# Kernel tuning notes

Hardware: AMD Instinct MI355X
Metric: run time of the kernel (lower is better)

## Reference

```python
import jax, jax.numpy as jnp
import numpy as np

B, T, U = 4, 500, 100
D = 512   # d_model
H = 512   # d_hidden
L = 2     # num_layers
V = 64    # len(phonemes)


def setup_inputs() -> dict:
    key = jax.random.key(0)
    ks = jax.random.split(key, 14)
    g = lambda k, shp: (jax.random.normal(k, shp, jnp.float32) * 0.05)
    return {
        "input_ids": jax.random.randint(ks[0], (B, U), 0, V),
        "memory": jax.random.normal(ks[1], (B, T, D), jnp.float32),
        "emb": g(ks[2], (V, D)),
        # stacked per-layer LSTM params (torch layout: [4H, in], gate order i,f,g,o)
        "w_ih": g(ks[3], (L, 4 * H, D)),
        "w_hh": g(ks[4], (L, 4 * H, H)),
        "b_ih": g(ks[5], (L, 4 * H)),
        "b_hh": g(ks[6], (L, 4 * H)),
        "fc_w": g(ks[7], (D, H)),     # torch Linear [out, in]
        "fc_b": g(ks[8], (D,)),
        "jw1": g(ks[9], (H, 2 * D)),  # Joint.forward_layer
        "jb1": g(ks[10], (H,)),
        "jw2": g(ks[11], (V, H)),     # Joint.project_layer
        "jb2": g(ks[12], (V,)),
    }


def _lstm_layer(x, wi, wh, bi, bh):
    # x: [B, U, in] -> returns ([B, U, H], h_T [B,H], c_T [B,H])
    b = x.shape[0]
    h0 = jnp.zeros((b, H), x.dtype)
    c0 = jnp.zeros((b, H), x.dtype)
    bias = bi + bh

    def step(carry, xt):
        h, c = carry
        gates = xt @ wi.T + h @ wh.T + bias  # [B, 4H]
        i, f, g, o = jnp.split(gates, 4, axis=-1)
        c = jax.nn.sigmoid(f) * c + jax.nn.sigmoid(i) * jnp.tanh(g)
        h = jax.nn.sigmoid(o) * jnp.tanh(c)
        return (h, c), h

    (hT, cT), ys = jax.lax.scan(step, (h0, c0), jnp.swapaxes(x, 0, 1))
    return jnp.swapaxes(ys, 0, 1), hT, cT


def reference(input_ids, memory, emb, w_ih, w_hh, b_ih, b_hh, fc_w, fc_b, jw1, jb1, jw2, jb2):
    # embedding lookup
    x = emb[input_ids]  # [B, U, D]
    hs, cs = [], []
    for l in range(L):
        x, hT, cT = _lstm_layer(x, w_ih[l], w_hh[l], b_ih[l], b_hh[l])
        hs.append(hT)
        cs.append(cT)
    h = jnp.stack(hs)  # [L, B, H]
    c = jnp.stack(cs)
    x = x @ fc_w.T + fc_b  # [B, U, D]

    # Joint: linear over concat(enc, dec) == split-weight broadcast add (same math)
    we = jw1[:, :D]  # acts on enc_state
    wd = jw1[:, D:]  # acts on dec_state
    enc_p = jnp.einsum("btd,hd->bth", memory, we)  # [B, T, H]
    dec_p = jnp.einsum("bud,hd->buh", x, wd)       # [B, U, H]
    joint_h = jnp.tanh(enc_p[:, :, None, :] + dec_p[:, None, :, :] + jb1)  # [B,T,U,H]
    out = jnp.einsum("btuh,vh->btuv", joint_h, jw2) + jb2  # [B, T, U, V]
    return out, h, c
```

## Files before the change

### kernel.cpp

```cpp
#include <hip/hip_runtime.h>

#define Bc 4
#define Tc 500
#define Uc 100
#define Vc 64
#define G4 2048

typedef __attribute__((ext_vector_type(8))) short short8v;
typedef __attribute__((ext_vector_type(4))) float f32x4;
typedef _Float16 h2v __attribute__((ext_vector_type(2)));

__device__ __forceinline__ float fsig(float x) {
  return __builtin_amdgcn_rcpf(1.f + __expf(-x));
}
__device__ __forceinline__ float ftanh(float x) {
  float e = __expf(2.f * x);
  return 1.f - 2.f * __builtin_amdgcn_rcpf(e + 1.f);
}
__device__ __forceinline__ short f2bf(float f) {
  unsigned u = __float_as_uint(f);
  unsigned r = (u + 0x7FFFu + ((u >> 16) & 1u)) >> 16;
  return (short)r;
}

__device__ __forceinline__ unsigned ldA(const unsigned* p) {
  return __hip_atomic_load(p, __ATOMIC_RELAXED, __HIP_MEMORY_SCOPE_AGENT);
}
__device__ __forceinline__ void stA(unsigned* p, unsigned v) {
  __hip_atomic_store(p, v, __ATOMIC_RELAXED, __HIP_MEMORY_SCOPE_AGENT);
}

template <int ATOMICST>
__device__ __forceinline__ void gemm_tile(
    const float* __restrict__ A, int lda,
    const float* __restrict__ Bw, int ldb,
    const float* __restrict__ bias, const float* __restrict__ bias2,
    float* __restrict__ C, int ldc, int N, int m0, int n0,
    const int* __restrict__ ids, const float* __restrict__ emb)
{
  __shared__ float As[16][65];
  __shared__ float Bs[16][65];
  const int tid = threadIdx.x;
  const int tx = tid & 15, ty = tid >> 4;
  float acc[4][4] = {};
  for (int k0 = 0; k0 < 512; k0 += 16) {
#pragma unroll
    for (int i = 0; i < 4; ++i) {
      int n = n0 + ty + 16 * i;
      float av = 0.f;
      if (n < N) {
        const float* ar = ids ? (emb + (long)ids[n] * 512) : (A + (long)n * lda);
        av = ar[k0 + tx];
      }
      As[tx][ty + 16 * i] = av;
      Bs[tx][ty + 16 * i] = Bw[(long)(m0 + ty + 16 * i) * ldb + k0 + tx];
    }
    __syncthreads();
#pragma unroll
    for (int kl = 0; kl < 16; ++kl) {
      float a[4], b[4];
#pragma unroll
      for (int i = 0; i < 4; ++i) a[i] = As[kl][ty * 4 + i];
#pragma unroll
      for (int j = 0; j < 4; ++j) b[j] = Bs[kl][tx * 4 + j];
#pragma unroll
      for (int i = 0; i < 4; ++i)
#pragma unroll
        for (int j = 0; j < 4; ++j) acc[i][j] += a[i] * b[j];
    }
    __syncthreads();
  }
#pragma unroll
  for (int i = 0; i < 4; ++i) {
    int n = n0 + ty * 4 + i;
    if (n >= N) continue;
#pragma unroll
    for (int j = 0; j < 4; ++j) {
      int m = m0 + tx * 4 + j;
      float v = acc[i][j];
      if (bias)  v += bias[m];
      if (bias2) v += bias2[m];
      if (ATOMICST)
        stA((unsigned*)C + (long)n * ldc + m, __float_as_uint(v));
      else
        C[(long)n * ldc + m] = v;
    }
  }
}

__device__ void wdc_tile(const float* __restrict__ jw1,
                         const float* __restrict__ fc_w,
                         float* __restrict__ wdc, int n0, int m0)
{
  __shared__ float As[16][65];
  __shared__ float Bs[16][65];
  const int tid = threadIdx.x;
  const int tx = tid & 15, ty = tid >> 4;
  float acc[4][4] = {};
  for (int k0 = 0; k0 < 512; k0 += 16) {
#pragma unroll
    for (int i = 0; i < 4; ++i) {
      As[tx][ty + 16 * i] = jw1[(long)(n0 + ty + 16 * i) * 1024 + 512 + k0 + tx];
      Bs[ty][tx + 16 * i] = fc_w[(long)(k0 + ty) * 512 + m0 + tx + 16 * i];
    }
    __syncthreads();
#pragma unroll
    for (int kl = 0; kl < 16; ++kl) {
      float a[4], b[4];
#pragma unroll
      for (int i = 0; i < 4; ++i) a[i] = As[kl][ty * 4 + i];
#pragma unroll
      for (int j = 0; j < 4; ++j) b[j] = Bs[kl][tx * 4 + j];
#pragma unroll
      for (int i = 0; i < 4; ++i)
#pragma unroll
        for (int j = 0; j < 4; ++j) acc[i][j] += a[i] * b[j];
    }
    __syncthreads();
  }
#pragma unroll
  for (int i = 0; i < 4; ++i)
#pragma unroll
    for (int j = 0; j < 4; ++j)
      stA((unsigned*)wdc + (long)(n0 + ty * 4 + i) * 512 + m0 + tx * 4 + j,
          __float_as_uint(acc[i][j]));
}

__device__ void dec_tile(const float* __restrict__ h1s, const float* __restrict__ wdc,
                         const float* __restrict__ jw1, const float* __restrict__ fc_b,
                         const float* __restrict__ jb1, float* __restrict__ decb,
                         const int* __restrict__ f1, int m0, int n0)
{
  __shared__ float As[16][65];
  __shared__ float Bs[16][65];
  __shared__ float biasl[64];
  const int tid = threadIdx.x;
  const int tx = tid & 15, ty = tid >> 4;
  int u_hi = 0;
  for (int rr = 0; rr < 64; ++rr) {
    int r = n0 + rr;
    if (r < 400) { int u = r % Uc; u_hi = max(u_hi, u + 1); }
  }
  if (tid < 32)
    while ((int)ldA((const unsigned*)(f1 + tid * 16)) < u_hi)
      __builtin_amdgcn_s_sleep(8);
  if (tid < 64) {
    int m = m0 + tid;
    const float4* wp = (const float4*)(jw1 + (long)m * 1024 + 512);
    const float4* fb = (const float4*)fc_b;
    float bb = jb1[m];
#pragma unroll 8
    for (int d4 = 0; d4 < 128; ++d4) {
      float4 w = wp[d4], f = fb[d4];
      bb += w.x * f.x + w.y * f.y + w.z * f.z + w.w * f.w;
    }
    biasl[tid] = bb;
  }
  __syncthreads();
  const unsigned* h1u = (const unsigned*)h1s;
  const unsigned* wdu = (const unsigned*)wdc;
  float acc[4][4] = {};
  for (int k0 = 0; k0 < 512; k0 += 16) {
    unsigned uA[4], uB[4];
#pragma unroll
    for (int i = 0; i < 4; ++i) {
      int n = n0 + ty + 16 * i;
      uA[i] = (n < 400) ? ldA(h1u + (long)(n % Uc) * G4 + (n / Uc) * 512 + k0 + tx) : 0u;
      uB[i] = ldA(wdu + (long)(m0 + ty + 16 * i) * 512 + k0 + tx);
    }
#pragma unroll
    for (int i = 0; i < 4; ++i) {
      int n = n0 + ty + 16 * i;
      while (uA[i] == 0xFFFFFFFFu)
        uA[i] = ldA(h1u + (long)(n % Uc) * G4 + (n / Uc) * 512 + k0 + tx);
      while (uB[i] == 0xFFFFFFFFu)
        uB[i] = ldA(wdu + (long)(m0 + ty + 16 * i) * 512 + k0 + tx);
      As[tx][ty + 16 * i] = __uint_as_float(uA[i]);
      Bs[tx][ty + 16 * i] = __uint_as_float(uB[i]);
    }
    __syncthreads();
#pragma unroll
    for (int kl = 0; kl < 16; ++kl) {
      float a[4], b[4];
#pragma unroll
      for (int i = 0; i < 4; ++i) a[i] = As[kl][ty * 4 + i];
#pragma unroll
      for (int j = 0; j < 4; ++j) b[j] = Bs[kl][tx * 4 + j];
#pragma unroll
      for (int i = 0; i < 4; ++i)
#pragma unroll
        for (int j = 0; j < 4; ++j) acc[i][j] += a[i] * b[j];
    }
    __syncthreads();
  }
#pragma unroll
  for (int i = 0; i < 4; ++i) {
    int n = n0 + ty * 4 + i;
    if (n >= 400) continue;
#pragma unroll
    for (int j = 0; j < 4; ++j)
      stA((unsigned*)decb + (long)n * 512 + m0 + tx * 4 + j,
          __float_as_uint(acc[i][j] + biasl[tx * 4 + j]));
  }
}

__device__ void rec_path(
    const float* __restrict__ ixp0,
    const float* __restrict__ wih1, const float* __restrict__ whh0,
    const float* __restrict__ whh1,
    const float* __restrict__ bih1, const float* __restrict__ bhh1,
    unsigned* __restrict__ h0s16, unsigned* __restrict__ h1s16,
    float* __restrict__ h1s32,
    float* __restrict__ hO, float* __restrict__ cO, int* __restrict__ flags)
{
  __shared__ unsigned hl[2048];
  __shared__ float4 red4[512];
  const int tid = threadIdx.x;
  const int blk = blockIdx.x;
  const bool isL1 = blk >= 16;
  const int jb = blk - 16;
  const int rg = tid & 15, ks = tid >> 4;
  const int lane = tid & 63, wv = tid >> 6;
  int* f1 = flags + 512;

  h2v wr[8][16];
#pragma unroll
  for (int r = 0; r < 8; ++r) {
    int lr = rg * 8 + r;
    const float* wsrc; int grow;
    if (!isL1) { int q = lr >> 5, uu = lr & 31; grow = q * 512 + blk * 32 + uu; wsrc = whh0; }
    else {
      if (lr < 64) { int q = lr >> 4, uu = lr & 15; grow = q * 512 + jb * 16 + uu; wsrc = wih1; }
      else { int l2 = lr - 64; int q = l2 >> 4, uu = l2 & 15; grow = q * 512 + jb * 16 + uu; wsrc = whh1; }
    }
    const float* wp = wsrc + (long)grow * 512 + ks * 32;
#pragma unroll
    for (int jj = 0; jj < 16; ++jj) {
      h2v t; t[0] = (_Float16)wp[2 * jj]; t[1] = (_Float16)wp[2 * jj + 1];
      wr[r][jj] = t;
    }
  }

  const int npair = isL1 ? 8 : 16;
  const bool eact = tid < npair * 4;
  const int ep = tid >> 2, eb = tid & 3;
  float creg[2] = {0.f, 0.f};
  float bgate[2][4];
  if (isL1 && eact) {
#pragma unroll
    for (int o = 0; o < 2; ++o)
#pragma unroll
      for (int q = 0; q < 4; ++q) {
        int grow = q * 512 + jb * 16 + 2 * ep + o;
        bgate[o][q] = bih1[grow] + bhh1[grow];
      }
  }

  const unsigned* ixu = (const unsigned*)ixp0;
  const int hsrc = (isL1 && rg >= 8) ? 1 : 0;
  const float* redf = (const float*)red4;

  for (int s = 0; s < Uc; ++s) {
    unsigned ha[4] = {0u, 0u, 0u, 0u}, hb[4] = {0u, 0u, 0u, 0u};
    const unsigned* pa = nullptr; const unsigned* pb = nullptr;
    if (!isL1) { if (s > 0) pa = h0s16 + (long)(s - 1) * 1024 + tid * 4; }
    else {
      pa = h0s16 + (long)s * 1024 + tid * 4;
      if (s > 0) pb = h1s16 + (long)(s - 1) * 1024 + tid * 4;
    }
    if (pa) {
#pragma unroll
      for (int c = 0; c < 4; ++c) ha[c] = ldA(pa + c);
    }
    if (pb) {
#pragma unroll
      for (int c = 0; c < 4; ++c) hb[c] = ldA(pb + c);
    }

    float ixv[2][4] = {};
    if (!isL1 && eact) {
      const unsigned* ib = ixu + ((long)(eb * Uc + s) * G4 + blk * 32 + 2 * ep);
#pragma unroll
      for (int o = 0; o < 2; ++o)
#pragma unroll
        for (int q = 0; q < 4; ++q) {
          unsigned g = ldA(ib + o + q * 512);
          while (g == 0xFFFFFFFFu) { __builtin_amdgcn_s_sleep(1); g = ldA(ib + o + q * 512); }
          ixv[o][q] = __uint_as_float(g);
        }
    }

    if (pa) {
#pragma unroll
      for (int c = 0; c < 4; ++c)
        while (ha[c] == 0xFFFFFFFFu) { __builtin_amdgcn_s_sleep(1); ha[c] = ldA(pa + c); }
    }
    if (pb) {
#pragma unroll
      for (int c = 0; c < 4; ++c)
        while (hb[c] == 0xFFFFFFFFu) { __builtin_amdgcn_s_sleep(1); hb[c] = ldA(pb + c); }
    }

    *(uint4*)&hl[tid * 4] = make_uint4(ha[0], ha[1], ha[2], ha[3]);
    if (isL1)
      *(uint4*)&hl[1024 + tid * 4] = make_uint4(hb[0], hb[1], hb[2], hb[3]);
    __syncthreads();

    float acc[8][4] = {};
    const unsigned* hbase = &hl[hsrc * 1024 + ks * 16];
#pragma unroll
    for (int jw = 0; jw < 4; ++jw) {
      unsigned q[4][4];
#pragma unroll
      for (int b = 0; b < 4; ++b) {
        uint4 t = *(const uint4*)&hbase[b * 256 + jw * 4];
        q[b][0] = t.x; q[b][1] = t.y; q[b][2] = t.z; q[b][3] = t.w;
      }
#pragma unroll
      for (int r = 0; r < 8; ++r)
#pragma unroll
        for (int w = 0; w < 4; ++w) {
          h2v wv2 = wr[r][jw * 4 + w];
#pragma unroll
          for (int b = 0; b < 4; ++b)
            acc[r][b] = __builtin_amdgcn_fdot2(
                wv2, __builtin_bit_cast(h2v, q[b][w]), acc[r][b], false);
        }
    }
#pragma unroll
    for (int r = 0; r < 8; ++r)
#pragma unroll
      for (int b = 0; b < 4; ++b) {
        float v = acc[r][b];
        v += __shfl_xor(v, 16);
        v += __shfl_xor(v, 32);
        acc[r][b] = v;
      }
    if (lane < 16) {
#pragma unroll
      for (int r = 0; r < 8; ++r)
        red4[wv * 128 + lane * 8 + r] =
            make_float4(acc[r][0], acc[r][1], acc[r][2], acc[r][3]);
    }
    __syncthreads();

    if (eact) {
      float hn2[2], cn2[2];
#pragma unroll
      for (int o = 0; o < 2; ++o) {
        int uu = 2 * ep + o;
        float gv[4];
#pragma unroll
        for (int q = 0; q < 4; ++q) {
          int lrA = isL1 ? (q * 16 + uu) : (q * 32 + uu);
          float sv = 0.f;
#pragma unroll
          for (int w = 0; w < 4; ++w)
            sv += redf[(w * 128 + (lrA >> 3) * 8 + (lrA & 7)) * 4 + eb];
          if (isL1) {
            int lrB = 64 + q * 16 + uu;
#pragma unroll
            for (int w = 0; w < 4; ++w)
              sv += redf[(w * 128 + (lrB >> 3) * 8 + (lrB & 7)) * 4 + eb];
            sv += bgate[o][q];
          } else {
            sv += ixv[o][q];
          }
          gv[q] = sv;
        }
        float cn = fsig(gv[1]) * creg[o] + fsig(gv[0]) * ftanh(gv[2]);
        float hn = fsig(gv[3]) * ftanh(cn);
        creg[o] = cn;
        hn2[o] = hn; cn2[o] = cn;
      }
      int gu = (isL1 ? jb * 16 : blk * 32) + 2 * ep;
      h2v hp; hp[0] = (_Float16)hn2[0]; hp[1] = (_Float16)hn2[1];
      unsigned pw = __builtin_bit_cast(unsigned, hp);
      stA((isL1 ? h1s16 : h0s16) + (long)s * 1024 + eb * 256 + (gu >> 1), pw);
      if (isL1) {
        unsigned* d32 = (unsigned*)h1s32 + (long)s * G4 + eb * 512 + gu;
        stA(d32, __float_as_uint(hn2[0]));
        stA(d32 + 1, __float_as_uint(hn2[1]));
      }
      if (s == Uc - 1) {
#pragma unroll
        for (int o = 0; o < 2; ++o) {
          hO[(isL1 ? G4 : 0) + eb * 512 + gu + o] = hn2[o];
          cO[(isL1 ? G4 : 0) + eb * 512 + gu + o] = cn2[o];
        }
      }
      if (isL1 && tid == 0) stA((unsigned*)(f1 + jb * 16), (unsigned)(s + 1));
    }
  }
}

__global__ __launch_bounds__(256, 1) void k_fused(
    const int* __restrict__ ids, const float* __restrict__ emb,
    const float* __restrict__ memory,
    const float* __restrict__ w_ih, const float* __restrict__ b_ih,
    const float* __restrict__ b_hh,
    const float* __restrict__ wih1, const float* __restrict__ whh0,
    const float* __restrict__ whh1,
    const float* __restrict__ bih1, const float* __restrict__ bhh1,
    const float* __restrict__ jw1, const float* __restrict__ jb1,
    const float* __restrict__ fc_w, const float* __restrict__ fc_b,
    float* __restrict__ ixp0, unsigned* __restrict__ h0s16,
    unsigned* __restrict__ h1s16, float* __restrict__ h1s32,
    float* __restrict__ wdc, float* __restrict__ decb, float* __restrict__ encb,
    float* __restrict__ hO, float* __restrict__ cO, int* __restrict__ flags)
{
  const int blk = blockIdx.x;
  if (blk < 48) {
    rec_path(ixp0, wih1, whh0, whh1, bih1, bhh1, h0s16, h1s16, h1s32,
             hO, cO, flags);
  } else if (blk < 272) {
    static const int nt_ord[7] = {0, 1, 3, 4, 2, 5, 6};
    int g = blk - 48;
    gemm_tile<1>(nullptr, 0, w_ih, 512, b_ih, b_hh,
                 ixp0, G4, Bc * Uc, (g % 32) * 64, nt_ord[g / 32] * 64, ids, emb);
  } else if (blk < 336) {
    int g = blk - 272;
    wdc_tile(jw1, fc_w, wdc, (g & 7) * 64, (g >> 3) * 64);
  } else if (blk < 592) {
    int g = blk - 336;
    gemm_tile<0>(memory, 512, jw1, 1024, nullptr, nullptr,
                 encb, 512, Bc * Tc, (g & 7) * 64, (g >> 3) * 64, nullptr, nullptr);
  } else {
    int g = blk - 592;
    dec_tile(h1s32, wdc, jw1, fc_b, jb1, decb, flags + 512, (g & 7) * 64, (g >> 3) * 64);
  }
}

__global__ __launch_bounds__(256) void k_jmfma(
    const float* __restrict__ enc, const float* __restrict__ dec,
    const float* __restrict__ jw2, const float* __restrict__ jb2,
    float* __restrict__ out)
{
  __shared__ float el[512];
  __shared__ short th[112][136];
  const int tid = threadIdx.x;
  const int lane = tid & 63, wv = tid >> 6;
  const int bt = blockIdx.x;
  const int b = bt / Tc;
  const int v0 = wv * 16;
  const int vl = lane & 15, kg = lane >> 4;

  short8v breg[16];
#pragma unroll
  for (int ksx = 0; ksx < 16; ++ksx) {
    const float* wp = jw2 + (long)(v0 + vl) * 512 + ksx * 32 + kg * 8;
    float4 x0 = *(const float4*)wp;
    float4 x1 = *(const float4*)(wp + 4);
    short8v t;
    t[0] = f2bf(x0.x); t[1] = f2bf(x0.y); t[2] = f2bf(x0.z); t[3] = f2bf(x0.w);
    t[4] = f2bf(x1.x); t[5] = f2bf(x1.y); t[6] = f2bf(x1.z); t[7] = f2bf(x1.w);
    breg[ksx] = t;
  }
  const float jbv = jb2[v0 + vl];
  for (int i = tid; i < 512; i += 256) el[i] = enc[(long)bt * 512 + i];

  f32x4 acc[7];
#pragma unroll
  for (int ut = 0; ut < 7; ++ut) acc[ut] = (f32x4){0.f, 0.f, 0.f, 0.f};
  __syncthreads();

  const float* dec0 = dec + (long)b * Uc * 512;
  for (int kc = 0; kc < 4; ++kc) {
#pragma unroll 5
    for (int it = 0; it < 50; ++it) {
      int flat = it * 256 + tid;
      int u = flat >> 7, kk = flat & 127;
      float dv = dec0[(long)u * 512 + kc * 128 + kk];
      th[u][kk] = f2bf(ftanh(el[kc * 128 + kk] + dv));
    }
    __syncthreads();
#pragma unroll
    for (int ks4 = 0; ks4 < 4; ++ks4) {
      int ko = ks4 * 32 + kg * 8;
#pragma unroll
      for (int ut = 0; ut < 7; ++ut) {
        short8v a = *(const short8v*)&th[ut * 16 + vl][ko];
        acc[ut] = __builtin_amdgcn_mfma_f32_16x16x32_bf16(a, breg[kc * 4 + ks4],
                                                          acc[ut], 0, 0, 0);
      }
    }
    __syncthreads();
  }
#pragma unroll
  for (int ut = 0; ut < 7; ++ut) {
#pragma unroll
    for (int i = 0; i < 4; ++i) {
      int u = ut * 16 + kg * 4 + i;
      if (u < Uc)
        out[((long)bt * Uc + u) * 64 + v0 + vl] = acc[ut][i] + jbv;
    }
  }
}

extern "C" void kernel_launch(void* const* d_in, const int* in_sizes, int n_in,
                              void* d_out, int out_size, void* d_ws, size_t ws_size,
                              hipStream_t stream)
{
  const int*   ids    = (const int*)d_in[0];
  const float* memory = (const float*)d_in[1];
  const float* emb    = (const float*)d_in[2];
  const float* w_ih   = (const float*)d_in[3];
  const float* w_hh   = (const float*)d_in[4];
  const float* b_ih   = (const float*)d_in[5];
  const float* b_hh   = (const float*)d_in[6];
  const float* fc_w   = (const float*)d_in[7];
  const float* fc_b   = (const float*)d_in[8];
  const float* jw1    = (const float*)d_in[9];
  const float* jb1    = (const float*)d_in[10];
  const float* jw2    = (const float*)d_in[11];
  const float* jb2    = (const float*)d_in[12];
  float* out = (float*)d_out;

  float* wsf = (float*)d_ws;
  int*      flags = (int*)d_ws;
  float*    ixp0  = wsf + 4096;
  unsigned* h0s16 = (unsigned*)(wsf + 823296);
  unsigned* h1s16 = (unsigned*)(wsf + 925696);
  float*    h1s32 = wsf + 1028096;
  float*    wdc   = wsf + 1232896;
  float*    decb  = wsf + 1495040;
  float*    encb  = wsf + 1699840;

  float* hO = out + (long)Bc * Tc * Uc * Vc;
  float* cO = hO + 2 * Bc * 512;

  hipMemsetAsync(flags, 0, 4096 * 4, stream);
  hipMemsetAsync(ixp0, 0xFF, (size_t)(1699840 - 4096) * 4, stream);

  k_fused<<<648, 256, 0, stream>>>(ids, emb, memory,
                                   w_ih, b_ih, b_hh,
                                   w_ih + (long)G4 * 512,
                                   w_hh,
                                   w_hh + (long)G4 * 512,
                                   b_ih + G4, b_hh + G4,
                                   jw1, jb1, fc_w, fc_b,
                                   ixp0, h0s16, h1s16, h1s32, wdc, decb, encb,
                                   hO, cO, flags);

  k_jmfma<<<2000, 256, 0, stream>>>(encb, decb, jw2, jb2, out);
}
```

Baseline: 774.6 us.

## Halve recurrent LSTM block count, spill extra weight rows to shared memory

Shrinks the persistent LSTM recurrence from 48 to 24 blocks, so each block handles twice as many hidden units. Each thread now owns 16 fp16 weight rows: 10 stay in registers and 6 live in a large shared-memory buffer. Fewer blocks mean fewer participants in each cross-block step handshake, which should cut per-timestep synchronization latency. In exchange, each block does twice the per-step dot-product work and reads shared memory, and the single big shared allocation (used by every role in the fused kernel) may limit how many GEMM blocks fit on a CU.

```diff
diff --git a/kernel.cpp b/kernel.cpp
--- a/kernel.cpp
+++ b/kernel.cpp
@@ -10,6 +10,11 @@
 typedef __attribute__((ext_vector_type(4))) float f32x4;
 typedef _Float16 h2v __attribute__((ext_vector_type(2)));
 
+#define SMEM_BYTES 124416
+#define WL_WORDS_STRIDE 260
+#define HL_OFF 99840
+#define RED_OFF 108032
+
 __device__ __forceinline__ float fsig(float x) {
   return __builtin_amdgcn_rcpf(1.f + __expf(-x));
 }
@@ -32,14 +37,15 @@
 
 template <int ATOMICST>
 __device__ __forceinline__ void gemm_tile(
+    char* smem,
     const float* __restrict__ A, int lda,
     const float* __restrict__ Bw, int ldb,
     const float* __restrict__ bias, const float* __restrict__ bias2,
     float* __restrict__ C, int ldc, int N, int m0, int n0,
     const int* __restrict__ ids, const float* __restrict__ emb)
 {
-  __shared__ float As[16][65];
-  __shared__ float Bs[16][65];
+  float (*As)[65] = (float (*)[65])smem;
+  float (*Bs)[65] = (float (*)[65])(smem + 4160);
   const int tid = threadIdx.x;
   const int tx = tid & 15, ty = tid >> 4;
   float acc[4][4] = {};
@@ -88,12 +94,13 @@
   }
 }
 
-__device__ void wdc_tile(const float* __restrict__ jw1,
+__device__ void wdc_tile(char* smem,
+                         const float* __restrict__ jw1,
                          const float* __restrict__ fc_w,
                          float* __restrict__ wdc, int n0, int m0)
 {
-  __shared__ float As[16][65];
-  __shared__ float Bs[16][65];
+  float (*As)[65] = (float (*)[65])smem;
+  float (*Bs)[65] = (float (*)[65])(smem + 4160);
   const int tid = threadIdx.x;
   const int tx = tid & 15, ty = tid >> 4;
   float acc[4][4] = {};
@@ -126,14 +133,15 @@
           __float_as_uint(acc[i][j]));
 }
 
-__device__ void dec_tile(const float* __restrict__ h1s, const float* __restrict__ wdc,
+__device__ void dec_tile(char* smem,
+                         const float* __restrict__ h1s, const float* __restrict__ wdc,
                          const float* __restrict__ jw1, const float* __restrict__ fc_b,
                          const float* __restrict__ jb1, float* __restrict__ decb,
                          const int* __restrict__ f1, int m0, int n0)
 {
-  __shared__ float As[16][65];
-  __shared__ float Bs[16][65];
-  __shared__ float biasl[64];
+  float (*As)[65] = (float (*)[65])smem;
+  float (*Bs)[65] = (float (*)[65])(smem + 4160);
+  float* biasl = (float*)(smem + 8320);
   const int tid = threadIdx.x;
   const int tx = tid & 15, ty = tid >> 4;
   int u_hi = 0;
@@ -141,7 +149,7 @@
     int r = n0 + rr;
     if (r < 400) { int u = r % Uc; u_hi = max(u_hi, u + 1); }
   }
-  if (tid < 32)
+  if (tid < 16)
     while ((int)ldA((const unsigned*)(f1 + tid * 16)) < u_hi)
       __builtin_amdgcn_s_sleep(8);
   if (tid < 64) {
@@ -205,6 +213,7 @@
 }
 
 __device__ void rec_path(
+    char* smem,
     const float* __restrict__ ixp0,
     const float* __restrict__ wih1, const float* __restrict__ whh0,
     const float* __restrict__ whh1,
@@ -213,35 +222,39 @@
     float* __restrict__ h1s32,
     float* __restrict__ hO, float* __restrict__ cO, int* __restrict__ flags)
 {
-  __shared__ unsigned hl[2048];
-  __shared__ float4 red4[512];
+  unsigned* wlu = (unsigned*)smem;
+  unsigned* hl  = (unsigned*)(smem + HL_OFF);
+  float*    redf = (float*)(smem + RED_OFF);
   const int tid = threadIdx.x;
   const int blk = blockIdx.x;
-  const bool isL1 = blk >= 16;
-  const int jb = blk - 16;
+  const bool isL1 = blk >= 8;
+  const int jb = blk - 8;
   const int rg = tid & 15, ks = tid >> 4;
   const int lane = tid & 63, wv = tid >> 6;
   int* f1 = flags + 512;
 
-  h2v wr[8][16];
-#pragma unroll
-  for (int r = 0; r < 8; ++r) {
-    int lr = rg * 8 + r;
+  h2v wr[10][16];
+  unsigned* wlp = wlu + (rg * 6) * WL_WORDS_STRIDE + ks * 16;
+#pragma unroll
+  for (int r = 0; r < 16; ++r) {
+    int lr = rg * 16 + r;
     const float* wsrc; int grow;
-    if (!isL1) { int q = lr >> 5, uu = lr & 31; grow = q * 512 + blk * 32 + uu; wsrc = whh0; }
+    if (!isL1) { int q = lr >> 6, uu = lr & 63; grow = q * 512 + blk * 64 + uu; wsrc = whh0; }
     else {
-      if (lr < 64) { int q = lr >> 4, uu = lr & 15; grow = q * 512 + jb * 16 + uu; wsrc = wih1; }
-      else { int l2 = lr - 64; int q = l2 >> 4, uu = l2 & 15; grow = q * 512 + jb * 16 + uu; wsrc = whh1; }
+      int half = lr >> 7, rem = lr & 127;
+      int q = rem >> 5, uu = rem & 31;
+      grow = q * 512 + jb * 32 + uu; wsrc = half ? whh1 : wih1;
     }
     const float* wp = wsrc + (long)grow * 512 + ks * 32;
 #pragma unroll
     for (int jj = 0; jj < 16; ++jj) {
       h2v t; t[0] = (_Float16)wp[2 * jj]; t[1] = (_Float16)wp[2 * jj + 1];
-      wr[r][jj] = t;
-    }
-  }
-
-  const int npair = isL1 ? 8 : 16;
+      if (r < 10) wr[r][jj] = t;
+      else        wlp[(r - 10) * WL_WORDS_STRIDE + jj] = __builtin_bit_cast(unsigned, t);
+    }
+  }
+
+  const int npair = isL1 ? 16 : 32;
   const bool eact = tid < npair * 4;
   const int ep = tid >> 2, eb = tid & 3;
   float creg[2] = {0.f, 0.f};
@@ -251,14 +264,13 @@
     for (int o = 0; o < 2; ++o)
 #pragma unroll
       for (int q = 0; q < 4; ++q) {
-        int grow = q * 512 + jb * 16 + 2 * ep + o;
+        int grow = q * 512 + jb * 32 + 2 * ep + o;
         bgate[o][q] = bih1[grow] + bhh1[grow];
       }
   }
 
   const unsigned* ixu = (const unsigned*)ixp0;
   const int hsrc = (isL1 && rg >= 8) ? 1 : 0;
-  const float* redf = (const float*)red4;
 
   for (int s = 0; s < Uc; ++s) {
     unsigned ha[4] = {0u, 0u, 0u, 0u}, hb[4] = {0u, 0u, 0u, 0u};
@@ -279,7 +291,7 @@
 
     float ixv[2][4] = {};
     if (!isL1 && eact) {
-      const unsigned* ib = ixu + ((long)(eb * Uc + s) * G4 + blk * 32 + 2 * ep);
+      const unsigned* ib = ixu + ((long)(eb * Uc + s) * G4 + blk * 64 + 2 * ep);
 #pragma unroll
       for (int o = 0; o < 2; ++o)
 #pragma unroll
@@ -306,41 +318,48 @@
       *(uint4*)&hl[1024 + tid * 4] = make_uint4(hb[0], hb[1], hb[2], hb[3]);
     __syncthreads();
 
-    float acc[8][4] = {};
     const unsigned* hbase = &hl[hsrc * 1024 + ks * 16];
 #pragma unroll
-    for (int jw = 0; jw < 4; ++jw) {
-      unsigned q[4][4];
-#pragma unroll
-      for (int b = 0; b < 4; ++b) {
-        uint4 t = *(const uint4*)&hbase[b * 256 + jw * 4];
-        q[b][0] = t.x; q[b][1] = t.y; q[b][2] = t.z; q[b][3] = t.w;
-      }
-#pragma unroll
-      for (int r = 0; r < 8; ++r)
-#pragma unroll
-        for (int w = 0; w < 4; ++w) {
-          h2v wv2 = wr[r][jw * 4 + w];
-#pragma unroll
-          for (int b = 0; b < 4; ++b)
-            acc[r][b] = __builtin_amdgcn_fdot2(
-                wv2, __builtin_bit_cast(h2v, q[b][w]), acc[r][b], false);
+    for (int p = 0; p < 2; ++p) {
+      float acc[16][2] = {};
+#pragma unroll
+      for (int jw = 0; jw < 4; ++jw) {
+        uint4 t0 = *(const uint4*)&hbase[(2 * p) * 256 + jw * 4];
+        uint4 t1 = *(const uint4*)&hbase[(2 * p + 1) * 256 + jw * 4];
+        unsigned qb0[4] = {t0.x, t0.y, t0.z, t0.w};
+        unsigned qb1[4] = {t1.x, t1.y, t1.z, t1.w};
+#pragma unroll
+        for (int r = 0; r < 16; ++r) {
+          h2v wv2[4];
+          if (r < 10) {
+#pragma unroll
+            for (int w = 0; w < 4; ++w) wv2[w] = wr[r][jw * 4 + w];
+          } else {
+            uint4 wt = *(const uint4*)&wlp[(r - 10) * WL_WORDS_STRIDE + jw * 4];
+            wv2[0] = __builtin_bit_cast(h2v, wt.x);
+            wv2[1] = __builtin_bit_cast(h2v, wt.y);
+            wv2[2] = __builtin_bit_cast(h2v, wt.z);
+            wv2[3] = __builtin_bit_cast(h2v, wt.w);
+          }
+#pragma unroll
+          for (int w = 0; w < 4; ++w) {
+            acc[r][0] = __builtin_amdgcn_fdot2(
+                wv2[w], __builtin_bit_cast(h2v, qb0[w]), acc[r][0], false);
+            acc[r][1] = __builtin_amdgcn_fdot2(
+                wv2[w], __builtin_bit_cast(h2v, qb1[w]), acc[r][1], false);
+          }
         }
-    }
-#pragma unroll
-    for (int r = 0; r < 8; ++r)
-#pragma unroll
-      for (int b = 0; b < 4; ++b) {
-        float v = acc[r][b];
-        v += __shfl_xor(v, 16);
-        v += __shfl_xor(v, 32);
-        acc[r][b] = v;
-      }
-    if (lane < 16) {
-#pragma unroll
-      for (int r = 0; r < 8; ++r)
-        red4[wv * 128 + lane * 8 + r] =
-            make_float4(acc[r][0], acc[r][1], acc[r][2], acc[r][3]);
+      }
+#pragma unroll
+      for (int r = 0; r < 16; ++r)
+#pragma unroll
+        for (int b2 = 0; b2 < 2; ++b2) {
+          float v = acc[r][b2];
+          v += __shfl_xor(v, 16);
+          v += __shfl_xor(v, 32);
+          if (lane < 16)
+            redf[((wv * 16 + lane) * 16 + r) * 4 + 2 * p + b2] = v;
+        }
     }
     __syncthreads();
 
@@ -352,19 +371,22 @@
         float gv[4];
 #pragma unroll
         for (int q = 0; q < 4; ++q) {
-          int lrA = isL1 ? (q * 16 + uu) : (q * 32 + uu);
           float sv = 0.f;
-#pragma unroll
-          for (int w = 0; w < 4; ++w)
-            sv += redf[(w * 128 + (lrA >> 3) * 8 + (lrA & 7)) * 4 + eb];
-          if (isL1) {
-            int lrB = 64 + q * 16 + uu;
+          if (!isL1) {
+            int lr = q * 64 + uu;
 #pragma unroll
             for (int w = 0; w < 4; ++w)
-              sv += redf[(w * 128 + (lrB >> 3) * 8 + (lrB & 7)) * 4 + eb];
+              sv += redf[((w * 16 + (lr >> 4)) * 16 + (lr & 15)) * 4 + eb];
+            sv += ixv[o][q];
+          } else {
+            int lrA = q * 32 + uu;
+            int lrB = 128 + q * 32 + uu;
+#pragma unroll
+            for (int w = 0; w < 4; ++w) {
+              sv += redf[((w * 16 + (lrA >> 4)) * 16 + (lrA & 15)) * 4 + eb];
+              sv += redf[((w * 16 + (lrB >> 4)) * 16 + (lrB & 15)) * 4 + eb];
+            }
             sv += bgate[o][q];
-          } else {
-            sv += ixv[o][q];
           }
           gv[q] = sv;
         }
@@ -373,7 +395,7 @@
         creg[o] = cn;
         hn2[o] = hn; cn2[o] = cn;
       }
-      int gu = (isL1 ? jb * 16 : blk * 32) + 2 * ep;
+      int gu = (isL1 ? jb * 32 : blk * 64) + 2 * ep;
       h2v hp; hp[0] = (_Float16)hn2[0]; hp[1] = (_Float16)hn2[1];
       unsigned pw = __builtin_bit_cast(unsigned, hp);
       stA((isL1 ? h1s16 : h0s16) + (long)s * 1024 + eb * 256 + (gu >> 1), pw);
@@ -391,6 +413,7 @@
       }
       if (isL1 && tid == 0) stA((unsigned*)(f1 + jb * 16), (unsigned)(s + 1));
     }
+    __syncthreads();
   }
 }
 
@@ -409,25 +432,27 @@
     float* __restrict__ wdc, float* __restrict__ decb, float* __restrict__ encb,
     float* __restrict__ hO, float* __restrict__ cO, int* __restrict__ flags)
 {
+  __shared__ __attribute__((aligned(16))) char smem[SMEM_BYTES];
   const int blk = blockIdx.x;
-  if (blk < 48) {
-    rec_path(ixp0, wih1, whh0, whh1, bih1, bhh1, h0s16, h1s16, h1s32,
+  if (blk < 24) {
+    rec_path(smem, ixp0, wih1, whh0, whh1, bih1, bhh1, h0s16, h1s16, h1s32,
              hO, cO, flags);
-  } else if (blk < 272) {
+  } else if (blk < 248) {
     static const int nt_ord[7] = {0, 1, 3, 4, 2, 5, 6};
-    int g = blk - 48;
-    gemm_tile<1>(nullptr, 0, w_ih, 512, b_ih, b_hh,
+    int g = blk - 24;
+    gemm_tile<1>(smem, nullptr, 0, w_ih, 512, b_ih, b_hh,
                  ixp0, G4, Bc * Uc, (g % 32) * 64, nt_ord[g / 32] * 64, ids, emb);
-  } else if (blk < 336) {
-    int g = blk - 272;
-    wdc_tile(jw1, fc_w, wdc, (g & 7) * 64, (g >> 3) * 64);
-  } else if (blk < 592) {
-    int g = blk - 336;
-    gemm_tile<0>(memory, 512, jw1, 1024, nullptr, nullptr,
+  } else if (blk < 312) {
+    int g = blk - 248;
+    wdc_tile(smem, jw1, fc_w, wdc, (g & 7) * 64, (g >> 3) * 64);
+  } else if (blk < 568) {
+    int g = blk - 312;
+    gemm_tile<0>(smem, memory, 512, jw1, 1024, nullptr, nullptr,
                  encb, 512, Bc * Tc, (g & 7) * 64, (g >> 3) * 64, nullptr, nullptr);
   } else {
-    int g = blk - 592;
-    dec_tile(h1s32, wdc, jw1, fc_b, jb1, decb, flags + 512, (g & 7) * 64, (g >> 3) * 64);
+    int g = blk - 568;
+    dec_tile(smem, h1s32, wdc, jw1, fc_b, jb1, decb, flags + 512,
+             (g & 7) * 64, (g >> 3) * 64);
   }
 }
 
@@ -532,7 +557,7 @@
   hipMemsetAsync(flags, 0, 4096 * 4, stream);
   hipMemsetAsync(ixp0, 0xFF, (size_t)(1699840 - 4096) * 4, stream);
 
-  k_fused<<<648, 256, 0, stream>>>(ids, emb, memory,
+  k_fused<<<624, 256, 0, stream>>>(ids, emb, memory,
                                    w_ih, b_ih, b_hh,
                                    w_ih + (long)G4 * 512,
                                    w_hh,
```

After: 1.515 ms. 1.96x slower.

## Pin recurrent blocks to one XCD and use L2-scope loads for h exchange

Applied to the files above, without the earlier changes.

Blocks now take roles dynamically through atomic tickets and read their XCC_ID so that all 48 recurrent LSTM blocks try to land on a single XCD. When all of them share an XCD, the hidden-state exchange switches to sc0 global loads and plain volatile stores instead of agent-scope atomics, aiming to keep the per-step handoff in the shared L2 rather than going further out. The input-projection values for the next step are also prefetched into registers. The cost is a spin-wait during role assignment, and correctness depends on assumptions about cache coherence within one XCD.

```diff
diff --git a/kernel.cpp b/kernel.cpp
--- a/kernel.cpp
+++ b/kernel.cpp
@@ -28,6 +28,21 @@
 }
 __device__ __forceinline__ void stA(unsigned* p, unsigned v) {
   __hip_atomic_store(p, v, __ATOMIC_RELAXED, __HIP_MEMORY_SCOPE_AGENT);
+}
+__device__ __forceinline__ unsigned ldL2(const unsigned* p) {
+  unsigned v;
+  asm volatile("global_load_dword %0, %1, off sc0\n\ts_waitcnt vmcnt(0)"
+               : "=v"(v) : "v"(p) : "memory");
+  return v;
+}
+__device__ __forceinline__ uint4 ldL2x4(const unsigned* p) {
+  uint4 v;
+  asm volatile("global_load_dwordx4 %0, %1, off sc0\n\ts_waitcnt vmcnt(0)"
+               : "=v"(v) : "v"(p) : "memory");
+  return v;
+}
+__device__ __forceinline__ void stL2(unsigned* p, unsigned v) {
+  *(volatile unsigned*)p = v;
 }
 
 template <int ATOMICST>
@@ -205,30 +220,43 @@
 }
 
 __device__ void rec_path(
+    int role,
     const float* __restrict__ ixp0,
     const float* __restrict__ wih1, const float* __restrict__ whh0,
     const float* __restrict__ whh1,
     const float* __restrict__ bih1, const float* __restrict__ bhh1,
     unsigned* __restrict__ h0s16, unsigned* __restrict__ h1s16,
     float* __restrict__ h1s32,
-    float* __restrict__ hO, float* __restrict__ cO, int* __restrict__ flags)
+    float* __restrict__ hO, float* __restrict__ cO,
+    int* __restrict__ flags, int* __restrict__ xtab)
 {
   __shared__ unsigned hl[2048];
   __shared__ float4 red4[512];
+  __shared__ int mode_s;
   const int tid = threadIdx.x;
-  const int blk = blockIdx.x;
-  const bool isL1 = blk >= 16;
-  const int jb = blk - 16;
+  const bool isL1 = role >= 16;
+  const int jb = role - 16;
   const int rg = tid & 15, ks = tid >> 4;
   const int lane = tid & 63, wv = tid >> 6;
   int* f1 = flags + 512;
 
+  if (tid < 64) {
+    int idx = (tid < 48) ? tid : 47;
+    unsigned v = ldA((const unsigned*)(xtab + idx * 16));
+    while (v == 0u) { __builtin_amdgcn_s_sleep(4); v = ldA((const unsigned*)(xtab + idx * 16)); }
+    unsigned v0 = __shfl(v, 0);
+    unsigned long long ball = __ballot(v == v0);
+    if (tid == 0) mode_s = (ball == ~0ull) ? 1 : 0;
+  }
+  __syncthreads();
+  const bool fastm = (mode_s != 0);
+
   h2v wr[8][16];
 #pragma unroll
   for (int r = 0; r < 8; ++r) {
     int lr = rg * 8 + r;
     const float* wsrc; int grow;
-    if (!isL1) { int q = lr >> 5, uu = lr & 31; grow = q * 512 + blk * 32 + uu; wsrc = whh0; }
+    if (!isL1) { int q = lr >> 5, uu = lr & 31; grow = q * 512 + role * 32 + uu; wsrc = whh0; }
     else {
       if (lr < 64) { int q = lr >> 4, uu = lr & 15; grow = q * 512 + jb * 16 + uu; wsrc = wih1; }
       else { int l2 = lr - 64; int q = l2 >> 4, uu = l2 & 15; grow = q * 512 + jb * 16 + uu; wsrc = whh1; }
@@ -259,6 +287,16 @@
   const unsigned* ixu = (const unsigned*)ixp0;
   const int hsrc = (isL1 && rg >= 8) ? 1 : 0;
   const float* redf = (const float*)red4;
+
+  unsigned ixn[8];
+  const unsigned* ib0 = (!isL1 && eact)
+      ? ixu + ((long)(eb * Uc) * G4 + role * 32 + 2 * ep) : nullptr;
+  if (ib0) {
+#pragma unroll
+    for (int o = 0; o < 2; ++o)
+#pragma unroll
+      for (int q = 0; q < 4; ++q) ixn[o * 4 + q] = ldA(ib0 + o + q * 512);
+  }
 
   for (int s = 0; s < Uc; ++s) {
     unsigned ha[4] = {0u, 0u, 0u, 0u}, hb[4] = {0u, 0u, 0u, 0u};
@@ -268,23 +306,28 @@
       pa = h0s16 + (long)s * 1024 + tid * 4;
       if (s > 0) pb = h1s16 + (long)(s - 1) * 1024 + tid * 4;
     }
-    if (pa) {
-#pragma unroll
-      for (int c = 0; c < 4; ++c) ha[c] = ldA(pa + c);
-    }
-    if (pb) {
-#pragma unroll
-      for (int c = 0; c < 4; ++c) hb[c] = ldA(pb + c);
+    if (fastm) {
+      if (pa) { uint4 t = ldL2x4(pa); ha[0] = t.x; ha[1] = t.y; ha[2] = t.z; ha[3] = t.w; }
+      if (pb) { uint4 t = ldL2x4(pb); hb[0] = t.x; hb[1] = t.y; hb[2] = t.z; hb[3] = t.w; }
+    } else {
+      if (pa) {
+#pragma unroll
+        for (int c = 0; c < 4; ++c) ha[c] = ldA(pa + c);
+      }
+      if (pb) {
+#pragma unroll
+        for (int c = 0; c < 4; ++c) hb[c] = ldA(pb + c);
+      }
     }
 
     float ixv[2][4] = {};
-    if (!isL1 && eact) {
-      const unsigned* ib = ixu + ((long)(eb * Uc + s) * G4 + blk * 32 + 2 * ep);
+    if (ib0) {
+      const unsigned* ib = ib0 + (long)s * G4;
 #pragma unroll
       for (int o = 0; o < 2; ++o)
 #pragma unroll
         for (int q = 0; q < 4; ++q) {
-          unsigned g = ldA(ib + o + q * 512);
+          unsigned g = ixn[o * 4 + q];
           while (g == 0xFFFFFFFFu) { __builtin_amdgcn_s_sleep(1); g = ldA(ib + o + q * 512); }
           ixv[o][q] = __uint_as_float(g);
         }
@@ -293,12 +336,26 @@
     if (pa) {
 #pragma unroll
       for (int c = 0; c < 4; ++c)
-        while (ha[c] == 0xFFFFFFFFu) { __builtin_amdgcn_s_sleep(1); ha[c] = ldA(pa + c); }
+        while (ha[c] == 0xFFFFFFFFu) {
+          __builtin_amdgcn_s_sleep(1);
+          ha[c] = fastm ? ldL2(pa + c) : ldA(pa + c);
+        }
     }
     if (pb) {
 #pragma unroll
       for (int c = 0; c < 4; ++c)
-        while (hb[c] == 0xFFFFFFFFu) { __builtin_amdgcn_s_sleep(1); hb[c] = ldA(pb + c); }
+        while (hb[c] == 0xFFFFFFFFu) {
+          __builtin_amdgcn_s_sleep(1);
+          hb[c] = fastm ? ldL2(pb + c) : ldA(pb + c);
+        }
+    }
+
+    if (ib0 && s + 1 < Uc) {
+      const unsigned* ibn = ib0 + (long)(s + 1) * G4;
+#pragma unroll
+      for (int o = 0; o < 2; ++o)
+#pragma unroll
+        for (int q = 0; q < 4; ++q) ixn[o * 4 + q] = ldA(ibn + o + q * 512);
     }
 
     *(uint4*)&hl[tid * 4] = make_uint4(ha[0], ha[1], ha[2], ha[3]);
@@ -373,10 +430,11 @@
         creg[o] = cn;
         hn2[o] = hn; cn2[o] = cn;
       }
-      int gu = (isL1 ? jb * 16 : blk * 32) + 2 * ep;
+      int gu = (isL1 ? jb * 16 : role * 32) + 2 * ep;
       h2v hp; hp[0] = (_Float16)hn2[0]; hp[1] = (_Float16)hn2[1];
       unsigned pw = __builtin_bit_cast(unsigned, hp);
-      stA((isL1 ? h1s16 : h0s16) + (long)s * 1024 + eb * 256 + (gu >> 1), pw);
+      unsigned* d16 = (isL1 ? h1s16 : h0s16) + (long)s * 1024 + eb * 256 + (gu >> 1);
+      if (fastm) stL2(d16, pw); else stA(d16, pw);
       if (isL1) {
         unsigned* d32 = (unsigned*)h1s32 + (long)s * G4 + eb * 512 + gu;
         stA(d32, __float_as_uint(hn2[0]));
@@ -409,24 +467,55 @@
     float* __restrict__ wdc, float* __restrict__ decb, float* __restrict__ encb,
     float* __restrict__ hO, float* __restrict__ cO, int* __restrict__ flags)
 {
-  const int blk = blockIdx.x;
-  if (blk < 48) {
-    rec_path(ixp0, wih1, whh0, whh1, bih1, bhh1, h0s16, h1s16, h1s32,
-             hO, cO, flags);
-  } else if (blk < 272) {
+  __shared__ int role_s[2];
+  int* rec_tk = flags + 1024;
+  int* wrk_tk = flags + 1040;
+  int* xtab   = flags + 1088;
+  if (threadIdx.x == 0) {
+    unsigned xcd;
+    asm volatile("s_getreg_b32 %0, hwreg(HW_REG_XCC_ID)" : "=s"(xcd));
+    xcd &= 7u;
+    int role = -1;
+    if (xcd == 0u) {
+      int r = __hip_atomic_fetch_add(rec_tk, 1, __ATOMIC_RELAXED, __HIP_MEMORY_SCOPE_AGENT);
+      if (r < 48) role = r;
+    } else {
+      for (int it = 0; it < 64; ++it) {
+        if ((int)ldA((const unsigned*)rec_tk) >= 48) break;
+        __builtin_amdgcn_s_sleep(8);
+      }
+      if ((int)ldA((const unsigned*)rec_tk) < 48) {
+        int r = __hip_atomic_fetch_add(rec_tk, 1, __ATOMIC_RELAXED, __HIP_MEMORY_SCOPE_AGENT);
+        if (r < 48) role = r;
+      }
+    }
+    int wrk = -1;
+    if (role < 0)
+      wrk = __hip_atomic_fetch_add(wrk_tk, 1, __ATOMIC_RELAXED, __HIP_MEMORY_SCOPE_AGENT);
+    else
+      stA((unsigned*)(xtab + role * 16), xcd + 1u);
+    role_s[0] = role; role_s[1] = wrk;
+  }
+  __syncthreads();
+  const int role = role_s[0];
+  const int w = role_s[1];
+
+  if (role >= 0) {
+    rec_path(role, ixp0, wih1, whh0, whh1, bih1, bhh1, h0s16, h1s16, h1s32,
+             hO, cO, flags, xtab);
+  } else if (w < 224) {
     static const int nt_ord[7] = {0, 1, 3, 4, 2, 5, 6};
-    int g = blk - 48;
     gemm_tile<1>(nullptr, 0, w_ih, 512, b_ih, b_hh,
-                 ixp0, G4, Bc * Uc, (g % 32) * 64, nt_ord[g / 32] * 64, ids, emb);
-  } else if (blk < 336) {
-    int g = blk - 272;
+                 ixp0, G4, Bc * Uc, (w % 32) * 64, nt_ord[w / 32] * 64, ids, emb);
+  } else if (w < 288) {
+    int g = w - 224;
     wdc_tile(jw1, fc_w, wdc, (g & 7) * 64, (g >> 3) * 64);
-  } else if (blk < 592) {
-    int g = blk - 336;
+  } else if (w < 544) {
+    int g = w - 288;
     gemm_tile<0>(memory, 512, jw1, 1024, nullptr, nullptr,
                  encb, 512, Bc * Tc, (g & 7) * 64, (g >> 3) * 64, nullptr, nullptr);
-  } else {
-    int g = blk - 592;
+  } else if (w < 600) {
+    int g = w - 544;
     dec_tile(h1s32, wdc, jw1, fc_b, jb1, decb, flags + 512, (g & 7) * 64, (g >> 3) * 64);
   }
 }
```

Result: slower. 832.8 us (+7.5%).

## Persist fused-kernel worker blocks over tiles and prefetch next-step input projections

Applied to the files above, without the earlier changes.

Shrinks the fused launch from 648 blocks to 256 and has the 208 non-recurrent blocks each loop over up to three tiles (ixp GEMM, wdc, encoder GEMM, decoder). All roles now share one 86016-byte shared buffer sized to force one block per CU. The layer-0 recurrent blocks also load the next step's input-projection values early so that load latency overlaps the current step. The aim is to keep the 48 spin-waiting recurrent blocks resident while cutting per-block launch overhead and exposed load latency in the serial loop. The trade-off is less parallelism for the GEMM tiles and a risk of serialising dependent work.

```diff
diff --git a/kernel.cpp b/kernel.cpp
--- a/kernel.cpp
+++ b/kernel.cpp
@@ -10,6 +10,8 @@
 typedef __attribute__((ext_vector_type(4))) float f32x4;
 typedef _Float16 h2v __attribute__((ext_vector_type(2)));
 
+#define SMEM_BYTES 86016
+
 __device__ __forceinline__ float fsig(float x) {
   return __builtin_amdgcn_rcpf(1.f + __expf(-x));
 }
@@ -32,14 +34,15 @@
 
 template <int ATOMICST>
 __device__ __forceinline__ void gemm_tile(
+    char* smem,
     const float* __restrict__ A, int lda,
     const float* __restrict__ Bw, int ldb,
     const float* __restrict__ bias, const float* __restrict__ bias2,
     float* __restrict__ C, int ldc, int N, int m0, int n0,
     const int* __restrict__ ids, const float* __restrict__ emb)
 {
-  __shared__ float As[16][65];
-  __shared__ float Bs[16][65];
+  float (*As)[65] = (float (*)[65])smem;
+  float (*Bs)[65] = (float (*)[65])(smem + 4160);
   const int tid = threadIdx.x;
   const int tx = tid & 15, ty = tid >> 4;
   float acc[4][4] = {};
@@ -88,12 +91,13 @@
   }
 }
 
-__device__ void wdc_tile(const float* __restrict__ jw1,
+__device__ void wdc_tile(char* smem,
+                         const float* __restrict__ jw1,
                          const float* __restrict__ fc_w,
                          float* __restrict__ wdc, int n0, int m0)
 {
-  __shared__ float As[16][65];
-  __shared__ float Bs[16][65];
+  float (*As)[65] = (float (*)[65])smem;
+  float (*Bs)[65] = (float (*)[65])(smem + 4160);
   const int tid = threadIdx.x;
   const int tx = tid & 15, ty = tid >> 4;
   float acc[4][4] = {};
@@ -126,14 +130,15 @@
           __float_as_uint(acc[i][j]));
 }
 
-__device__ void dec_tile(const float* __restrict__ h1s, const float* __restrict__ wdc,
+__device__ void dec_tile(char* smem,
+                         const float* __restrict__ h1s, const float* __restrict__ wdc,
                          const float* __restrict__ jw1, const float* __restrict__ fc_b,
                          const float* __restrict__ jb1, float* __restrict__ decb,
                          const int* __restrict__ f1, int m0, int n0)
 {
-  __shared__ float As[16][65];
-  __shared__ float Bs[16][65];
-  __shared__ float biasl[64];
+  float (*As)[65] = (float (*)[65])smem;
+  float (*Bs)[65] = (float (*)[65])(smem + 4160);
+  float* biasl = (float*)(smem + 8320);
   const int tid = threadIdx.x;
   const int tx = tid & 15, ty = tid >> 4;
   int u_hi = 0;
@@ -205,6 +210,7 @@
 }
 
 __device__ void rec_path(
+    char* smem, int role,
     const float* __restrict__ ixp0,
     const float* __restrict__ wih1, const float* __restrict__ whh0,
     const float* __restrict__ whh1,
@@ -213,12 +219,11 @@
     float* __restrict__ h1s32,
     float* __restrict__ hO, float* __restrict__ cO, int* __restrict__ flags)
 {
-  __shared__ unsigned hl[2048];
-  __shared__ float4 red4[512];
+  unsigned* hl = (unsigned*)smem;
+  float4* red4 = (float4*)(smem + 8192);
   const int tid = threadIdx.x;
-  const int blk = blockIdx.x;
-  const bool isL1 = blk >= 16;
-  const int jb = blk - 16;
+  const bool isL1 = role >= 16;
+  const int jb = role - 16;
   const int rg = tid & 15, ks = tid >> 4;
   const int lane = tid & 63, wv = tid >> 6;
   int* f1 = flags + 512;
@@ -228,7 +233,7 @@
   for (int r = 0; r < 8; ++r) {
     int lr = rg * 8 + r;
     const float* wsrc; int grow;
-    if (!isL1) { int q = lr >> 5, uu = lr & 31; grow = q * 512 + blk * 32 + uu; wsrc = whh0; }
+    if (!isL1) { int q = lr >> 5, uu = lr & 31; grow = q * 512 + role * 32 + uu; wsrc = whh0; }
     else {
       if (lr < 64) { int q = lr >> 4, uu = lr & 15; grow = q * 512 + jb * 16 + uu; wsrc = wih1; }
       else { int l2 = lr - 64; int q = l2 >> 4, uu = l2 & 15; grow = q * 512 + jb * 16 + uu; wsrc = whh1; }
@@ -259,6 +264,16 @@
   const unsigned* ixu = (const unsigned*)ixp0;
   const int hsrc = (isL1 && rg >= 8) ? 1 : 0;
   const float* redf = (const float*)red4;
+
+  unsigned ixn[8];
+  const unsigned* ib0 = (!isL1 && eact)
+      ? ixu + ((long)(eb * Uc) * G4 + role * 32 + 2 * ep) : nullptr;
+  if (ib0) {
+#pragma unroll
+    for (int o = 0; o < 2; ++o)
+#pragma unroll
+      for (int q = 0; q < 4; ++q) ixn[o * 4 + q] = ldA(ib0 + o + q * 512);
+  }
 
   for (int s = 0; s < Uc; ++s) {
     unsigned ha[4] = {0u, 0u, 0u, 0u}, hb[4] = {0u, 0u, 0u, 0u};
@@ -278,13 +293,13 @@
     }
 
     float ixv[2][4] = {};
-    if (!isL1 && eact) {
-      const unsigned* ib = ixu + ((long)(eb * Uc + s) * G4 + blk * 32 + 2 * ep);
+    if (ib0) {
+      const unsigned* ib = ib0 + (long)s * G4;
 #pragma unroll
       for (int o = 0; o < 2; ++o)
 #pragma unroll
         for (int q = 0; q < 4; ++q) {
-          unsigned g = ldA(ib + o + q * 512);
+          unsigned g = ixn[o * 4 + q];
           while (g == 0xFFFFFFFFu) { __builtin_amdgcn_s_sleep(1); g = ldA(ib + o + q * 512); }
           ixv[o][q] = __uint_as_float(g);
         }
@@ -299,6 +314,14 @@
 #pragma unroll
       for (int c = 0; c < 4; ++c)
         while (hb[c] == 0xFFFFFFFFu) { __builtin_amdgcn_s_sleep(1); hb[c] = ldA(pb + c); }
+    }
+
+    if (ib0 && s + 1 < Uc) {
+      const unsigned* ibn = ib0 + (long)(s + 1) * G4;
+#pragma unroll
+      for (int o = 0; o < 2; ++o)
+#pragma unroll
+        for (int q = 0; q < 4; ++q) ixn[o * 4 + q] = ldA(ibn + o + q * 512);
     }
 
     *(uint4*)&hl[tid * 4] = make_uint4(ha[0], ha[1], ha[2], ha[3]);
@@ -373,7 +396,7 @@
         creg[o] = cn;
         hn2[o] = hn; cn2[o] = cn;
       }
-      int gu = (isL1 ? jb * 16 : blk * 32) + 2 * ep;
+      int gu = (isL1 ? jb * 16 : role * 32) + 2 * ep;
       h2v hp; hp[0] = (_Float16)hn2[0]; hp[1] = (_Float16)hn2[1];
       unsigned pw = __builtin_bit_cast(unsigned, hp);
       stA((isL1 ? h1s16 : h0s16) + (long)s * 1024 + eb * 256 + (gu >> 1), pw);
@@ -409,25 +432,34 @@
     float* __restrict__ wdc, float* __restrict__ decb, float* __restrict__ encb,
     float* __restrict__ hO, float* __restrict__ cO, int* __restrict__ flags)
 {
+  __shared__ __attribute__((aligned(16))) char smem[SMEM_BYTES];
   const int blk = blockIdx.x;
   if (blk < 48) {
-    rec_path(ixp0, wih1, whh0, whh1, bih1, bhh1, h0s16, h1s16, h1s32,
-             hO, cO, flags);
-  } else if (blk < 272) {
-    static const int nt_ord[7] = {0, 1, 3, 4, 2, 5, 6};
-    int g = blk - 48;
-    gemm_tile<1>(nullptr, 0, w_ih, 512, b_ih, b_hh,
-                 ixp0, G4, Bc * Uc, (g % 32) * 64, nt_ord[g / 32] * 64, ids, emb);
-  } else if (blk < 336) {
-    int g = blk - 272;
-    wdc_tile(jw1, fc_w, wdc, (g & 7) * 64, (g >> 3) * 64);
-  } else if (blk < 592) {
-    int g = blk - 336;
-    gemm_tile<0>(memory, 512, jw1, 1024, nullptr, nullptr,
-                 encb, 512, Bc * Tc, (g & 7) * 64, (g >> 3) * 64, nullptr, nullptr);
-  } else {
-    int g = blk - 592;
-    dec_tile(h1s32, wdc, jw1, fc_b, jb1, decb, flags + 512, (g & 7) * 64, (g >> 3) * 64);
+    rec_path(smem, blk, ixp0, wih1, whh0, whh1, bih1, bhh1,
+             h0s16, h1s16, h1s32, hO, cO, flags);
+    return;
+  }
+  const int w = blk - 48;
+  static const int nt_ord[7] = {0, 1, 3, 4, 2, 5, 6};
+  for (int k = 0; k < 3; ++k) {
+    int t = w + 208 * k;
+    if (t >= 600) break;
+    if (k) __syncthreads();
+    if (t < 224) {
+      gemm_tile<1>(smem, nullptr, 0, w_ih, 512, b_ih, b_hh,
+                   ixp0, G4, Bc * Uc, (t % 32) * 64, nt_ord[t / 32] * 64, ids, emb);
+    } else if (t < 288) {
+      int g = t - 224;
+      wdc_tile(smem, jw1, fc_w, wdc, (g & 7) * 64, (g >> 3) * 64);
+    } else if (t < 544) {
+      int g = t - 288;
+      gemm_tile<0>(smem, memory, 512, jw1, 1024, nullptr, nullptr,
+                   encb, 512, Bc * Tc, (g & 7) * 64, (g >> 3) * 64, nullptr, nullptr);
+    } else {
+      int g = t - 544;
+      dec_tile(smem, h1s32, wdc, jw1, fc_b, jb1, decb, flags + 512,
+               (g & 7) * 64, (g >> 3) * 64);
+    }
   }
 }
 
@@ -532,7 +564,7 @@
   hipMemsetAsync(flags, 0, 4096 * 4, stream);
   hipMemsetAsync(ixp0, 0xFF, (size_t)(1699840 - 4096) * 4, stream);
 
-  k_fused<<<648, 256, 0, stream>>>(ids, emb, memory,
+  k_fused<<<256, 256, 0, stream>>>(ids, emb, memory,
                                    w_ih, b_ih, b_hh,
                                    w_ih + (long)G4 * 512,
                                    w_hh,
```

Result: faster. 706.7 us, median of 2 (-8.8%).
